# Kernel optimization log

Measured on AMD Instinct MI355X. Metric: run time of the kernel, lower is better.

The kernel has to match this reference:

```python
import jax, jax.numpy as jnp
import numpy as np

N_NODES = 100000
N_EDGES = 1600000
D = 128
N_LAYERS = 3
N_GRAPHS = 64
BN_EPS = 1e-5


def setup_inputs() -> dict:
    key = jax.random.key(0)
    ks = jax.random.split(key, 8)
    x = jax.random.normal(ks[0], (N_NODES, D), dtype=jnp.float32)
    edge_index = jax.random.randint(ks[1], (2, N_EDGES), 0, N_NODES, dtype=jnp.int64)
    batch = jnp.sort(jax.random.randint(ks[2], (N_NODES,), 0, N_GRAPHS, dtype=jnp.int64))
    scale = 1.0 / np.sqrt(D)
    W1 = jax.random.normal(ks[3], (N_LAYERS, D, D), dtype=jnp.float32) * scale
    W2 = jax.random.normal(ks[4], (N_LAYERS, D, D), dtype=jnp.float32) * scale
    g1 = jnp.ones((N_LAYERS, D), dtype=jnp.float32)
    b1 = jnp.zeros((N_LAYERS, D), dtype=jnp.float32)
    g2 = jnp.ones((N_LAYERS, D), dtype=jnp.float32)
    b2 = jnp.zeros((N_LAYERS, D), dtype=jnp.float32)
    eps = jnp.zeros((N_LAYERS,), dtype=jnp.float32)
    return {"x": x, "edge_index": edge_index, "batch": batch,
            "W1": W1, "g1": g1, "b1": b1, "W2": W2, "g2": g2, "b2": b2, "eps": eps}


def _batchnorm(z, gamma, beta):
    # BatchNorm1d in training mode: biased variance over the node dimension.
    mu = jnp.mean(z, axis=0, keepdims=True)
    var = jnp.mean(jnp.square(z - mu), axis=0, keepdims=True)
    return (z - mu) * jax.lax.rsqrt(var + BN_EPS) * gamma + beta


def reference(x, edge_index, batch, W1, g1, b1, W2, g2, b2, eps):
    src, dst = edge_index[0], edge_index[1]
    h = x
    for l in range(N_LAYERS):
        # GIN aggregation: sum of neighbor features via edge-index scatter-add
        agg = jax.ops.segment_sum(h[src], dst, num_segments=N_NODES)
        z = (1.0 + eps[l]) * h + agg
        # MLP: Linear(no bias) -> BN -> ReLU -> Linear(no bias) -> BN
        z = _batchnorm(z @ W1[l], g1[l], b1[l])
        z = jax.nn.relu(z)
        z = _batchnorm(z @ W2[l], g2[l], b2[l])
        h = jax.nn.relu(z)  # gnn_non_linear
    node_emb = h
    # mean readout per graph
    counts = jax.ops.segment_sum(jnp.ones((N_NODES,), dtype=h.dtype), batch, num_segments=N_GRAPHS)
    graph_sum = jax.ops.segment_sum(h, batch, num_segments=N_GRAPHS)
    graph_emb = graph_sum / jnp.maximum(counts, 1.0)[:, None]
    # emb_normalize -> F.normalize(p=2, dim=-1)
    graph_emb = graph_emb / jnp.maximum(jnp.linalg.norm(graph_emb, axis=-1, keepdims=True), 1e-12)
    return node_emb, graph_emb
```

## Files before the change

kernel.cpp:

```cpp
#include <hip/hip_runtime.h>

#define N_NODES 100000
#define N_EDGES 1600000
#define D 128
#define N_GRAPHS 64
#define BN_EPS 1e-5f
#define NSLICE 16

#define BNODES 256
#define NBUCK ((N_NODES + BNODES - 1) / BNODES)
#define EPB 8192
#define NABLK ((N_EDGES + EPB - 1) / EPB)

typedef short short8 __attribute__((ext_vector_type(8)));
typedef float f32x4 __attribute__((ext_vector_type(4)));

__device__ inline unsigned short f2bf(float f) {
  unsigned int u = __float_as_uint(f);
  u += 0x7fffu + ((u >> 16) & 1);
  return (unsigned short)(u >> 16);
}
__device__ inline float bf2f(unsigned short h) {
  return __uint_as_float(((unsigned int)h) << 16);
}
__device__ inline void unpack8(uint4 u, float* f) {
  f[0] = __uint_as_float(u.x << 16); f[1] = __uint_as_float(u.x & 0xffff0000u);
  f[2] = __uint_as_float(u.y << 16); f[3] = __uint_as_float(u.y & 0xffff0000u);
  f[4] = __uint_as_float(u.z << 16); f[5] = __uint_as_float(u.z & 0xffff0000u);
  f[6] = __uint_as_float(u.w << 16); f[7] = __uint_as_float(u.w & 0xffff0000u);
}
__device__ inline uint4 pack8(const float* f) {
  uint4 u;
  u.x = f2bf(f[0]) | ((unsigned)f2bf(f[1]) << 16);
  u.y = f2bf(f[2]) | ((unsigned)f2bf(f[3]) << 16);
  u.z = f2bf(f[4]) | ((unsigned)f2bf(f[5]) << 16);
  u.w = f2bf(f[6]) | ((unsigned)f2bf(f[7]) << 16);
  return u;
}

__global__ __launch_bounds__(256) void k_cast(const float* __restrict__ in,
                                              unsigned short* __restrict__ o) {
  long i = ((long)blockIdx.x * blockDim.x + threadIdx.x) * 8;
  if (i >= (long)N_NODES * D) return;
  float4 a = *(const float4*)(in + i);
  float4 b = *(const float4*)(in + i + 4);
  float f[8] = {a.x, a.y, a.z, a.w, b.x, b.y, b.z, b.w};
  *(uint4*)(o + i) = pack8(f);
}

__global__ __launch_bounds__(128) void k_wprep(const float* __restrict__ W1,
                                               const float* __restrict__ W2,
                                               unsigned short* __restrict__ Wt) {
  int m = blockIdx.x;
  int n = blockIdx.y;
  int k = threadIdx.x;
  int l = m >> 1, s = m & 1;
  const float* W = (s == 0 ? W1 : W2) + (size_t)l * D * D;
  Wt[((size_t)m * D + n) * D + k] = f2bf(W[(size_t)k * D + n]);
}

__global__ __launch_bounds__(256) void k_histb(const int* __restrict__ dst,
                                               int* __restrict__ ecount) {
  __shared__ int lh[NBUCK];
  const int t = threadIdx.x;
  const int e0 = blockIdx.x * EPB;
  const int e1 = min(e0 + EPB, N_EDGES);
  for (int i = t; i < NBUCK; i += 256) lh[i] = 0;
  __syncthreads();
  for (int e = e0 + t; e < e1; e += 256) atomicAdd(&lh[dst[e] >> 8], 1);
  __syncthreads();
  for (int i = t; i < NBUCK; i += 256)
    if (lh[i]) atomicAdd(&ecount[i], lh[i]);
}

__global__ __launch_bounds__(512) void k_scanb(const int* __restrict__ ecount,
                                               int* __restrict__ ebase,
                                               int* __restrict__ gcur) {
  __shared__ int ls[512];
  int t = threadIdx.x;
  int v = (t < NBUCK) ? ecount[t] : 0;
  ls[t] = v;
  __syncthreads();
  for (int o = 1; o < 512; o <<= 1) {
    int u = (t >= o) ? ls[t - o] : 0;
    __syncthreads();
    ls[t] += u;
    __syncthreads();
  }
  int ex = ls[t] - v;
  if (t < NBUCK) { ebase[t] = ex; gcur[t] = ex; }
  if (t == 0) ebase[NBUCK] = N_EDGES;
}

__global__ __launch_bounds__(256) void k_scatA(const int* __restrict__ ei,
                                               int* __restrict__ gcur,
                                               int2* __restrict__ pairs) {
  __shared__ int lh[NBUCK];
  __shared__ int lbase[NBUCK];
  const int t = threadIdx.x;
  const int e0 = blockIdx.x * EPB;
  const int e1 = min(e0 + EPB, N_EDGES);
  for (int i = t; i < NBUCK; i += 256) lh[i] = 0;
  __syncthreads();
  for (int e = e0 + t; e < e1; e += 256) atomicAdd(&lh[ei[N_EDGES + e] >> 8], 1);
  __syncthreads();
  for (int i = t; i < NBUCK; i += 256)
    lbase[i] = (lh[i] > 0) ? atomicAdd(&gcur[i], lh[i]) : 0;
  __syncthreads();
  for (int e = e0 + t; e < e1; e += 256) {
    int s = ei[e];
    int d = ei[N_EDGES + e];
    int p = atomicAdd(&lbase[d >> 8], 1);
    pairs[p] = make_int2(s, d);
  }
}

__global__ __launch_bounds__(256) void k_scatB(const int2* __restrict__ pairs,
                                               const int* __restrict__ ebase,
                                               int* __restrict__ off,
                                               int* __restrict__ esrc) {
  __shared__ int lcnt[BNODES];
  __shared__ int ls[256];
  const int t = threadIdx.x;
  const int b = blockIdx.x;
  const int nb0 = b * BNODES;
  const int nn = min(BNODES, N_NODES - nb0);
  const int s0 = ebase[b], s1 = ebase[b + 1];
  if (t < nn) lcnt[t] = 0;
  __syncthreads();
  for (int e = s0 + t; e < s1; e += 256) atomicAdd(&lcnt[pairs[e].y - nb0], 1);
  __syncthreads();
  int c0 = (t < nn) ? lcnt[t] : 0;
  ls[t] = c0;
  __syncthreads();
  for (int o = 1; o < 256; o <<= 1) {
    int u = (t >= o) ? ls[t - o] : 0;
    __syncthreads();
    ls[t] += u;
    __syncthreads();
  }
  int pre = ls[t] - c0;
  if (t < nn) {
    off[nb0 + t] = s0 + pre;
    lcnt[t] = s0 + pre;
  }
  __syncthreads();
  for (int e = s0 + t; e < s1; e += 256) {
    int2 p = pairs[e];
    int pos = atomicAdd(&lcnt[p.y - nb0], 1);
    esrc[pos] = p.x;
  }
  if (b == 0 && t == 0) off[N_NODES] = N_EDGES;
}

template <int MODE>
__global__ __launch_bounds__(256) void k_aggz(const unsigned short* __restrict__ h,
                                              const int* __restrict__ off,
                                              const int* __restrict__ esrc,
                                              const float* __restrict__ epsp,
                                              const float* __restrict__ sc,
                                              const float* __restrict__ tb,
                                              unsigned short* __restrict__ z) {
  const int lane = threadIdx.x & 63;
  const int n = blockIdx.x * 4 + (threadIdx.x >> 6);
  const int c = lane << 1;
  float S0 = 0.f, S1 = 0.f, T0 = 0.f, T1 = 0.f;
  if (MODE == 1) { S0 = sc[c]; S1 = sc[c + 1]; T0 = tb[c]; T1 = tb[c + 1]; }
  const float e = 1.0f + epsp[0];
  const int o0 = off[n], o1 = off[n + 1];

  float a0, a1;
  {
    unsigned int u = *(const unsigned int*)(h + (size_t)n * D + c);
    float lo = __uint_as_float(u << 16);
    float hi = __uint_as_float(u & 0xffff0000u);
    if (MODE == 1) {
      lo = fmaxf(fmaf(lo, S0, T0), 0.f);
      hi = fmaxf(fmaf(hi, S1, T1), 0.f);
    }
    a0 = e * lo;
    a1 = e * hi;
  }

  int j = o0;
  for (; j + 3 < o1; j += 4) {
    int i0 = esrc[j], i1 = esrc[j + 1], i2 = esrc[j + 2], i3 = esrc[j + 3];
    unsigned int u0 = *(const unsigned int*)(h + (size_t)i0 * D + c);
    unsigned int u1 = *(const unsigned int*)(h + (size_t)i1 * D + c);
    unsigned int u2 = *(const unsigned int*)(h + (size_t)i2 * D + c);
    unsigned int u3 = *(const unsigned int*)(h + (size_t)i3 * D + c);
    float l0 = __uint_as_float(u0 << 16), h0 = __uint_as_float(u0 & 0xffff0000u);
    float l1 = __uint_as_float(u1 << 16), h1 = __uint_as_float(u1 & 0xffff0000u);
    float l2 = __uint_as_float(u2 << 16), h2 = __uint_as_float(u2 & 0xffff0000u);
    float l3 = __uint_as_float(u3 << 16), h3 = __uint_as_float(u3 & 0xffff0000u);
    if (MODE == 1) {
      l0 = fmaxf(fmaf(l0, S0, T0), 0.f); h0 = fmaxf(fmaf(h0, S1, T1), 0.f);
      l1 = fmaxf(fmaf(l1, S0, T0), 0.f); h1 = fmaxf(fmaf(h1, S1, T1), 0.f);
      l2 = fmaxf(fmaf(l2, S0, T0), 0.f); h2 = fmaxf(fmaf(h2, S1, T1), 0.f);
      l3 = fmaxf(fmaf(l3, S0, T0), 0.f); h3 = fmaxf(fmaf(h3, S1, T1), 0.f);
    }
    a0 += (l0 + l1) + (l2 + l3);
    a1 += (h0 + h1) + (h2 + h3);
  }
  for (; j < o1; j++) {
    unsigned int u0 = *(const unsigned int*)(h + (size_t)esrc[j] * D + c);
    float l0 = __uint_as_float(u0 << 16), h0 = __uint_as_float(u0 & 0xffff0000u);
    if (MODE == 1) {
      l0 = fmaxf(fmaf(l0, S0, T0), 0.f);
      h0 = fmaxf(fmaf(h0, S1, T1), 0.f);
    }
    a0 += l0;
    a1 += h0;
  }
  unsigned int pk = (unsigned int)f2bf(a0) | ((unsigned int)f2bf(a1) << 16);
  *(unsigned int*)(z + (size_t)n * D + c) = pk;
}

template <int MODE>
__global__ __launch_bounds__(256) void k_gemm(const unsigned short* __restrict__ A,
                                              const unsigned short* __restrict__ Wt,
                                              unsigned short* __restrict__ out,
                                              const float* __restrict__ sc,
                                              const float* __restrict__ tb,
                                              float* __restrict__ ssum,
                                              float* __restrict__ ssq) {
  __shared__ unsigned short Zs[64 * 136];
  __shared__ float psum[16 * 128];
  __shared__ float psq[16 * 128];
  const int t = threadIdx.x;
  const int row0 = blockIdx.x * 64;

#pragma unroll
  for (int i = 0; i < 4; i++) {
    int q = t + i * 256;
    int r = q >> 4, cb = (q & 15) << 3;
    int grow = row0 + r;
    uint4 u = make_uint4(0u, 0u, 0u, 0u);
    if (grow < N_NODES) {
      u = *(const uint4*)(A + (size_t)grow * D + cb);
      if (MODE == 1) {
        float f[8];
        unpack8(u, f);
#pragma unroll
        for (int jj = 0; jj < 8; jj++)
          f[jj] = fmaxf(fmaf(f[jj], sc[cb + jj], tb[cb + jj]), 0.f);
        u = pack8(f);
      }
    }
    *(uint4*)&Zs[r * 136 + cb] = u;
  }
  __syncthreads();

  const int lane = t & 63;
  const int wave = t >> 6;
  const int quad = lane >> 4;
  const int lr = lane & 15;
  const int m0 = wave * 16;

  f32x4 acc[8];
#pragma unroll
  for (int i = 0; i < 8; i++) acc[i] = (f32x4){0.f, 0.f, 0.f, 0.f};

#pragma unroll
  for (int kc = 0; kc < 128; kc += 32) {
    short8 af = *(const short8*)&Zs[(m0 + lr) * 136 + kc + quad * 8];
#pragma unroll
    for (int nt = 0; nt < 8; nt++) {
      short8 bf = *(const short8*)(Wt + (size_t)(nt * 16 + lr) * D + kc + quad * 8);
      acc[nt] = __builtin_amdgcn_mfma_f32_16x16x32_bf16(af, bf, acc[nt], 0, 0, 0);
    }
  }

#pragma unroll
  for (int nt = 0; nt < 8; nt++) {
    int col = nt * 16 + lr;
    float s = acc[nt][0] + acc[nt][1] + acc[nt][2] + acc[nt][3];
    float qq = acc[nt][0] * acc[nt][0] + acc[nt][1] * acc[nt][1] +
               acc[nt][2] * acc[nt][2] + acc[nt][3] * acc[nt][3];
    int gi = (wave * 4 + quad) * 128 + col;
    psum[gi] = s;
    psq[gi] = qq;
  }

#pragma unroll
  for (int rr = 0; rr < 4; rr++) {
    int grow = row0 + m0 + quad * 4 + rr;
    if (grow < N_NODES) {
#pragma unroll
      for (int nt = 0; nt < 8; nt++)
        out[(size_t)grow * D + nt * 16 + lr] = f2bf(acc[nt][rr]);
    }
  }

  __syncthreads();
  if (t < 128) {
    float S = 0.f, Q = 0.f;
#pragma unroll
    for (int i = 0; i < 16; i++) {
      S += psum[i * 128 + t];
      Q += psq[i * 128 + t];
    }
    int slice = blockIdx.x & (NSLICE - 1);
    atomicAdd(&ssum[slice * 128 + t], S);
    atomicAdd(&ssq[slice * 128 + t], Q);
  }
}

__global__ void k_bnfin(const float* __restrict__ ssum, const float* __restrict__ ssq,
                        const float* __restrict__ gamma, const float* __restrict__ beta,
                        float* __restrict__ sc, float* __restrict__ tb) {
  int f = threadIdx.x;
  float S = 0.f, Q = 0.f;
  for (int i = 0; i < NSLICE; i++) { S += ssum[i * 128 + f]; Q += ssq[i * 128 + f]; }
  float m = S * (1.0f / (float)N_NODES);
  float v = Q * (1.0f / (float)N_NODES) - m * m;
  float r = rsqrtf(v + BN_EPS);
  float s = r * gamma[f];
  sc[f] = s;
  tb[f] = beta[f] - m * s;
}

#define RCH 64
__global__ __launch_bounds__(128) void k_readout(const unsigned short* __restrict__ y,
                                                 const int* __restrict__ batch,
                                                 const float* __restrict__ sc,
                                                 const float* __restrict__ tb,
                                                 float* __restrict__ node_out,
                                                 float* __restrict__ gsum,
                                                 int* __restrict__ gcnt) {
  int start = blockIdx.x * RCH;
  int end = min(start + RCH, N_NODES);
  if (start >= end) return;
  int f = threadIdx.x;
  float s = sc[f], tt = tb[f];
  float acc = 0.f;
  int cnt = 0;
  int curg = batch[start];
  for (int n = start; n < end; n++) {
    int gg = batch[n];
    float v = fmaxf(fmaf(bf2f(y[(size_t)n * D + f]), s, tt), 0.f);
    node_out[(size_t)n * D + f] = v;
    if (gg != curg) {
      atomicAdd(&gsum[curg * D + f], acc);
      if (f == 0) atomicAdd(&gcnt[curg], cnt);
      acc = 0.f; cnt = 0; curg = gg;
    }
    acc += v;
    cnt++;
  }
  atomicAdd(&gsum[curg * D + f], acc);
  if (f == 0) atomicAdd(&gcnt[curg], cnt);
}

__global__ __launch_bounds__(128) void k_gnorm(const float* __restrict__ gsum,
                                               const int* __restrict__ gcnt,
                                               float* __restrict__ out) {
  __shared__ float red[128];
  int g = blockIdx.x, f = threadIdx.x;
  float c = (float)gcnt[g];
  float v = gsum[g * D + f] / fmaxf(c, 1.0f);
  red[f] = v * v;
  __syncthreads();
  for (int o = 64; o > 0; o >>= 1) {
    if (f < o) red[f] += red[f + o];
    __syncthreads();
  }
  float nrm = sqrtf(red[0]);
  out[(size_t)g * D + f] = v / fmaxf(nrm, 1e-12f);
}

extern "C" void kernel_launch(void* const* d_in, const int* in_sizes, int n_in,
                              void* d_out, int out_size, void* d_ws, size_t ws_size,
                              hipStream_t stream) {
  const float* x   = (const float*)d_in[0];
  const int*   ei  = (const int*)d_in[1];
  const int*   bat = (const int*)d_in[2];
  const float* W1  = (const float*)d_in[3];
  const float* g1  = (const float*)d_in[4];
  const float* b1  = (const float*)d_in[5];
  const float* W2  = (const float*)d_in[6];
  const float* g2  = (const float*)d_in[7];
  const float* b2  = (const float*)d_in[8];
  const float* eps = (const float*)d_in[9];
  float* out = (float*)d_out;

  char* w = (char*)d_ws;
  const size_t FEAT_B = (size_t)N_NODES * D * 2;
  unsigned short* xb   = (unsigned short*)w; w += FEAT_B;
  unsigned short* bufA = (unsigned short*)w; w += FEAT_B;
  unsigned short* bufB = (unsigned short*)w; w += FEAT_B;
  unsigned short* bufC = (unsigned short*)w; w += FEAT_B;
  unsigned short* WtB  = (unsigned short*)w; w += (size_t)6 * D * D * 2;
  int* off   = (int*)w; w += 400016;
  int* ebase = (int*)w; w += 2048;
  int* gcur  = (int*)w; w += 2048;
  int* esrc  = (int*)w; w += (size_t)N_EDGES * 4;
  float* sc1 = (float*)w; w += 512;
  float* tb1 = (float*)w; w += 512;
  float* sc2 = (float*)w; w += 512;
  float* tb2 = (float*)w; w += 512;
  char* zreg = w;
  int* ecount  = (int*)w; w += 2048;
  float* stats = (float*)w; w += (size_t)6 * 2 * NSLICE * 128 * 4;
  float* gsum  = (float*)w; w += (size_t)N_GRAPHS * D * 4;
  int* gcnt    = (int*)w; w += 256;
  size_t zbytes = (size_t)((char*)w - zreg);
  int2* pairs = (int2*)bufB;

  hipMemsetAsync(zreg, 0, zbytes, stream);

  k_cast<<<(N_NODES * D / 8 + 255) / 256, 256, 0, stream>>>(x, xb);
  k_wprep<<<dim3(6, 128), 128, 0, stream>>>(W1, W2, WtB);

  k_histb<<<NABLK, 256, 0, stream>>>(ei + N_EDGES, ecount);
  k_scanb<<<1, 512, 0, stream>>>(ecount, ebase, gcur);
  k_scatA<<<NABLK, 256, 0, stream>>>(ei, gcur, pairs);
  k_scatB<<<NBUCK, 256, 0, stream>>>(pairs, ebase, off, esrc);

  const int gemm_grid = (N_NODES + 63) / 64;
  const int aggz_grid = N_NODES / 4;

  for (int l = 0; l < 3; l++) {
    float* s1 = stats + (size_t)(l * 2 + 0) * 2 * NSLICE * 128;
    float* q1 = s1 + NSLICE * 128;
    float* s2 = stats + (size_t)(l * 2 + 1) * 2 * NSLICE * 128;
    float* q2 = s2 + NSLICE * 128;
    if (l == 0) {
      k_aggz<0><<<aggz_grid, 256, 0, stream>>>(xb, off, esrc, eps + l,
                                               nullptr, nullptr, bufA);
    } else {
      k_aggz<1><<<aggz_grid, 256, 0, stream>>>(bufC, off, esrc, eps + l,
                                               sc2, tb2, bufA);
    }
    k_gemm<0><<<gemm_grid, 256, 0, stream>>>(bufA, WtB + (size_t)(l * 2 + 0) * D * D, bufB,
                                             nullptr, nullptr, s1, q1);
    k_bnfin<<<1, 128, 0, stream>>>(s1, q1, g1 + (size_t)l * D, b1 + (size_t)l * D, sc1, tb1);
    k_gemm<1><<<gemm_grid, 256, 0, stream>>>(bufB, WtB + (size_t)(l * 2 + 1) * D * D, bufC,
                                             sc1, tb1, s2, q2);
    k_bnfin<<<1, 128, 0, stream>>>(s2, q2, g2 + (size_t)l * D, b2 + (size_t)l * D, sc2, tb2);
  }

  k_readout<<<(N_NODES + RCH - 1) / RCH, 128, 0, stream>>>(bufC, bat, sc2, tb2,
                                                           out, gsum, gcnt);
  k_gnorm<<<N_GRAPHS, 128, 0, stream>>>(gsum, gcnt, out + (size_t)N_NODES * D);
}
```

Baseline: 654.9 us.

## Materialize BN+ReLU activations and gather 16-byte rows with 4 edges per wave

The aggregation kernel now has each quarter-wave read a full 16-byte chunk of a neighbor row, so four edges are processed in parallel per wave and combined with cross-lane shuffles. This replaces the previous 4-byte-per-lane gathers. The BN+ReLU transform of the previous layer is moved out of the gather loop into a separate elementwise kernel that writes the activated features once. This removes the per-edge FMA/max work and widens memory transactions, at the cost of an extra full read/write pass over the node features each layer.

```diff
diff --git a/kernel.cpp b/kernel.cpp
--- a/kernel.cpp
+++ b/kernel.cpp
@@ -153,67 +153,68 @@
   if (b == 0 && t == 0) off[N_NODES] = N_EDGES;
 }
 
-template <int MODE>
 __global__ __launch_bounds__(256) void k_aggz(const unsigned short* __restrict__ h,
                                               const int* __restrict__ off,
                                               const int* __restrict__ esrc,
                                               const float* __restrict__ epsp,
-                                              const float* __restrict__ sc,
-                                              const float* __restrict__ tb,
                                               unsigned short* __restrict__ z) {
   const int lane = threadIdx.x & 63;
   const int n = blockIdx.x * 4 + (threadIdx.x >> 6);
-  const int c = lane << 1;
-  float S0 = 0.f, S1 = 0.f, T0 = 0.f, T1 = 0.f;
-  if (MODE == 1) { S0 = sc[c]; S1 = sc[c + 1]; T0 = tb[c]; T1 = tb[c + 1]; }
+  const int es = lane >> 4;
+  const int fl = lane & 15;
+  const int c = fl << 3;
   const float e = 1.0f + epsp[0];
   const int o0 = off[n], o1 = off[n + 1];
 
-  float a0, a1;
+  float acc[8];
+#pragma unroll
+  for (int q = 0; q < 8; q++) acc[q] = 0.f;
+
+  int j = o0;
+  for (; j + 4 <= o1; j += 4) {
+    int s = esrc[j + es];
+    uint4 u = *(const uint4*)(h + (size_t)s * D + c);
+    float f[8];
+    unpack8(u, f);
+#pragma unroll
+    for (int q = 0; q < 8; q++) acc[q] += f[q];
+  }
+  if (es < o1 - j) {
+    int s = esrc[j + es];
+    uint4 u = *(const uint4*)(h + (size_t)s * D + c);
+    float f[8];
+    unpack8(u, f);
+#pragma unroll
+    for (int q = 0; q < 8; q++) acc[q] += f[q];
+  }
+#pragma unroll
+  for (int q = 0; q < 8; q++) {
+    acc[q] += __shfl_xor(acc[q], 16, 64);
+    acc[q] += __shfl_xor(acc[q], 32, 64);
+  }
   {
-    unsigned int u = *(const unsigned int*)(h + (size_t)n * D + c);
-    float lo = __uint_as_float(u << 16);
-    float hi = __uint_as_float(u & 0xffff0000u);
-    if (MODE == 1) {
-      lo = fmaxf(fmaf(lo, S0, T0), 0.f);
-      hi = fmaxf(fmaf(hi, S1, T1), 0.f);
-    }
-    a0 = e * lo;
-    a1 = e * hi;
-  }
-
-  int j = o0;
-  for (; j + 3 < o1; j += 4) {
-    int i0 = esrc[j], i1 = esrc[j + 1], i2 = esrc[j + 2], i3 = esrc[j + 3];
-    unsigned int u0 = *(const unsigned int*)(h + (size_t)i0 * D + c);
-    unsigned int u1 = *(const unsigned int*)(h + (size_t)i1 * D + c);
-    unsigned int u2 = *(const unsigned int*)(h + (size_t)i2 * D + c);
-    unsigned int u3 = *(const unsigned int*)(h + (size_t)i3 * D + c);
-    float l0 = __uint_as_float(u0 << 16), h0 = __uint_as_float(u0 & 0xffff0000u);
-    float l1 = __uint_as_float(u1 << 16), h1 = __uint_as_float(u1 & 0xffff0000u);
-    float l2 = __uint_as_float(u2 << 16), h2 = __uint_as_float(u2 & 0xffff0000u);
-    float l3 = __uint_as_float(u3 << 16), h3 = __uint_as_float(u3 & 0xffff0000u);
-    if (MODE == 1) {
-      l0 = fmaxf(fmaf(l0, S0, T0), 0.f); h0 = fmaxf(fmaf(h0, S1, T1), 0.f);
-      l1 = fmaxf(fmaf(l1, S0, T0), 0.f); h1 = fmaxf(fmaf(h1, S1, T1), 0.f);
-      l2 = fmaxf(fmaf(l2, S0, T0), 0.f); h2 = fmaxf(fmaf(h2, S1, T1), 0.f);
-      l3 = fmaxf(fmaf(l3, S0, T0), 0.f); h3 = fmaxf(fmaf(h3, S1, T1), 0.f);
-    }
-    a0 += (l0 + l1) + (l2 + l3);
-    a1 += (h0 + h1) + (h2 + h3);
-  }
-  for (; j < o1; j++) {
-    unsigned int u0 = *(const unsigned int*)(h + (size_t)esrc[j] * D + c);
-    float l0 = __uint_as_float(u0 << 16), h0 = __uint_as_float(u0 & 0xffff0000u);
-    if (MODE == 1) {
-      l0 = fmaxf(fmaf(l0, S0, T0), 0.f);
-      h0 = fmaxf(fmaf(h0, S1, T1), 0.f);
-    }
-    a0 += l0;
-    a1 += h0;
-  }
-  unsigned int pk = (unsigned int)f2bf(a0) | ((unsigned int)f2bf(a1) << 16);
-  *(unsigned int*)(z + (size_t)n * D + c) = pk;
+    uint4 u = *(const uint4*)(h + (size_t)n * D + c);
+    float f[8];
+    unpack8(u, f);
+#pragma unroll
+    for (int q = 0; q < 8; q++) acc[q] = fmaf(e, f[q], acc[q]);
+  }
+  if (es == 0) *(uint4*)(z + (size_t)n * D + c) = pack8(acc);
+}
+
+__global__ __launch_bounds__(256) void k_ew(const unsigned short* __restrict__ y,
+                                            const float* __restrict__ sc,
+                                            const float* __restrict__ tb,
+                                            unsigned short* __restrict__ o) {
+  long i = ((long)blockIdx.x * 256 + threadIdx.x) * 8;
+  if (i >= (long)N_NODES * D) return;
+  int cb = (int)(i & 127);
+  uint4 u = *(const uint4*)(y + i);
+  float f[8];
+  unpack8(u, f);
+#pragma unroll
+  for (int q = 0; q < 8; q++) f[q] = fmaxf(fmaf(f[q], sc[cb + q], tb[cb + q]), 0.f);
+  *(uint4*)(o + i) = pack8(f);
 }
 
 template <int MODE>
@@ -419,19 +420,17 @@
 
   const int gemm_grid = (N_NODES + 63) / 64;
   const int aggz_grid = N_NODES / 4;
+  const int ew_grid = (N_NODES * D / 8 + 255) / 256;
 
   for (int l = 0; l < 3; l++) {
     float* s1 = stats + (size_t)(l * 2 + 0) * 2 * NSLICE * 128;
     float* q1 = s1 + NSLICE * 128;
     float* s2 = stats + (size_t)(l * 2 + 1) * 2 * NSLICE * 128;
     float* q2 = s2 + NSLICE * 128;
-    if (l == 0) {
-      k_aggz<0><<<aggz_grid, 256, 0, stream>>>(xb, off, esrc, eps + l,
-                                               nullptr, nullptr, bufA);
-    } else {
-      k_aggz<1><<<aggz_grid, 256, 0, stream>>>(bufC, off, esrc, eps + l,
-                                               sc2, tb2, bufA);
-    }
+    if (l > 0) {
+      k_ew<<<ew_grid, 256, 0, stream>>>(bufC, sc2, tb2, xb);
+    }
+    k_aggz<<<aggz_grid, 256, 0, stream>>>(xb, off, esrc, eps + l, bufA);
     k_gemm<0><<<gemm_grid, 256, 0, stream>>>(bufA, WtB + (size_t)(l * 2 + 0) * D * D, bufB,
                                              nullptr, nullptr, s1, q1);
     k_bnfin<<<1, 128, 0, stream>>>(s1, q1, g1 + (size_t)l * D, b1 + (size_t)l * D, sc1, tb1);
```

Measured after the change: 661.8 us. About the same (+1.1%).
